# Performance work log

Measured on AMD Instinct MI355X. Metric: run time of the kernel, lower is better.

## Reference

```python
import jax, jax.numpy as jnp
import numpy as np
import math

D_MODEL = 1024
NUM_HEADS = 16
NUM_LAYERS = 4
D_FF = 4096
TEXT_DIM = 512
B, SV, ST = 4, 2048, 100
EPS = 1e-5


def positional_encoding(seq_len, d):
    pos = jnp.arange(seq_len, dtype=jnp.float32)[:, None]
    div = jnp.exp(jnp.arange(0, d, 2, dtype=jnp.float32) * (-math.log(10000.0) / d))
    pe = jnp.zeros((seq_len, d), dtype=jnp.float32)
    pe = pe.at[:, 0::2].set(jnp.sin(pos * div))
    pe = pe.at[:, 1::2].set(jnp.cos(pos * div))
    return pe  # [seq_len, d]


def layer_norm(x, g, b):
    mu = jnp.mean(x, axis=-1, keepdims=True)
    var = jnp.mean(jnp.square(x - mu), axis=-1, keepdims=True)
    return (x - mu) * jax.lax.rsqrt(var + EPS) * g + b


def setup_inputs() -> dict:
    key = jax.random.key(0)
    ks = jax.random.split(key, 24)
    s = 0.02
    inp = {
        "video": jax.random.normal(ks[0], (B, SV, D_MODEL), jnp.float32),
        "text": jax.random.normal(ks[1], (B, ST, TEXT_DIM), jnp.float32),
        "text_mask": jnp.ones((B, ST), jnp.int32),
        # stacked per-layer params, weights stored [in, out]
        "Wq_w": jax.random.normal(ks[2], (NUM_LAYERS, D_MODEL, D_MODEL)) * s,
        "Wq_b": jnp.zeros((NUM_LAYERS, D_MODEL)),
        "Wk_w": jax.random.normal(ks[3], (NUM_LAYERS, TEXT_DIM, D_MODEL)) * s,
        "Wk_b": jnp.zeros((NUM_LAYERS, D_MODEL)),
        "Wv_w": jax.random.normal(ks[4], (NUM_LAYERS, TEXT_DIM, D_MODEL)) * s,
        "Wv_b": jnp.zeros((NUM_LAYERS, D_MODEL)),
        "Wo_w": jax.random.normal(ks[5], (NUM_LAYERS, D_MODEL, D_MODEL)) * s,
        "Wo_b": jnp.zeros((NUM_LAYERS, D_MODEL)),
        "fc1_w": jax.random.normal(ks[6], (NUM_LAYERS, D_MODEL, D_FF)) * s,
        "fc1_b": jnp.zeros((NUM_LAYERS, D_FF)),
        "fc2_w": jax.random.normal(ks[7], (NUM_LAYERS, D_FF, D_MODEL)) * s,
        "fc2_b": jnp.zeros((NUM_LAYERS, D_MODEL)),
        "n2_g": jnp.ones((NUM_LAYERS, D_MODEL)),
        "n2_b": jnp.zeros((NUM_LAYERS, D_MODEL)),
        "n3_g": jnp.ones((NUM_LAYERS, D_MODEL)),
        "n3_b": jnp.zeros((NUM_LAYERS, D_MODEL)),
    }
    return inp


def cross_attn_layer(video, text, mask, wq, bq, wk, bk, wv, bv, wo, bo):
    Bv, Sq, D = video.shape
    H, dk = NUM_HEADS, D_MODEL // NUM_HEADS
    q = (video @ wq + bq).reshape(Bv, Sq, H, dk).transpose(0, 2, 1, 3)  # bhqd
    k = (text @ wk + bk).reshape(Bv, -1, H, dk).transpose(0, 2, 1, 3)   # bhkd
    v = (text @ wv + bv).reshape(Bv, -1, H, dk).transpose(0, 2, 1, 3)
    scores = jnp.einsum("bhqd,bhkd->bhqk", q, k) / math.sqrt(dk)
    scores = jnp.where(mask, scores, jnp.float32(-1e9))
    probs = jax.nn.softmax(scores, axis=-1)
    out = jnp.einsum("bhqk,bhkd->bhqd", probs, v)
    out = out.transpose(0, 2, 1, 3).reshape(Bv, Sq, D)
    return out @ wo + bo


def reference(video, text, text_mask, Wq_w, Wq_b, Wk_w, Wk_b, Wv_w, Wv_b,
              Wo_w, Wo_b, fc1_w, fc1_b, fc2_w, fc2_b, n2_g, n2_b, n3_g, n3_b):
    video = video + positional_encoding(SV, D_MODEL)[None, :video.shape[1]]
    text = text + positional_encoding(ST, TEXT_DIM)[None, :text.shape[1]]
    mask = (text_mask != 0)[:, None, None, :]  # [B,1,1,St]
    for l in range(NUM_LAYERS):
        attn = cross_attn_layer(video, text, mask,
                                Wq_w[l], Wq_b[l], Wk_w[l], Wk_b[l],
                                Wv_w[l], Wv_b[l], Wo_w[l], Wo_b[l])
        video = layer_norm(video + attn, n2_g[l], n2_b[l])
        ff = jax.nn.relu(video @ fc1_w[l] + fc1_b[l]) @ fc2_w[l] + fc2_b[l]
        video = layer_norm(video + ff, n3_g[l], n3_b[l])
    return video
```

## Files before the change

### kernel.cpp

```cpp
#include <hip/hip_runtime.h>
#include <cstdint>
#include <cstddef>

typedef unsigned short u16;
typedef __attribute__((ext_vector_type(8))) __bf16 bf16x8;
typedef __attribute__((ext_vector_type(4))) float f32x4;

__device__ __forceinline__ f32x4 mfma_16x16x32(bf16x8 a, bf16x8 b, f32x4 c) {
  return __builtin_amdgcn_mfma_f32_16x16x32_bf16(a, b, c, 0, 0, 0);
}

__device__ __forceinline__ u16 f2bf(float f) {
  union { float f; uint32_t u; } c; c.f = f;
  uint32_t u = c.u + 0x7FFFu + ((c.u >> 16) & 1u);
  return (u16)(u >> 16);
}

__device__ __forceinline__ float bf2f(u16 x) {
  union { uint32_t u; float f; } c; c.u = ((uint32_t)x) << 16;
  return c.f;
}

__device__ __forceinline__ void gload_lds16(const void* g, void* l) {
  __builtin_amdgcn_global_load_lds(
      (__attribute__((address_space(1))) void*)(uintptr_t)g,
      (__attribute__((address_space(3))) void*)l, 16, 0, 0);
}

template<bool OUT_BF16, bool RELU, bool ACC>
__global__ __launch_bounds__(256, 2) void gemm_ring4(
    const u16* __restrict__ A, int lda, const u16* __restrict__ Bt, int ldb,
    const float* __restrict__ bias, void* Cout, int ldc,
    int M, int N, int K)
{
  constexpr int BM = 128, BN = 128;
  constexpr int SLOT = (BM + BN) * 32;
  __shared__ u16 ring[3 * SLOT];

  const int tid = threadIdx.x;
  const int lane = tid & 63, wave = tid >> 6;
  const int wm = wave >> 1, wn = wave & 1;
  const int m0 = blockIdx.x * BM, n0 = blockIdx.y * BN;

  const u16* gA[2];
  const u16* gB[2];
  #pragma unroll
  for (int i = 0; i < 2; i++) {
    int c = tid + i * 256, r = c >> 2;
    gA[i] = A + (size_t)(m0 + r) * lda + (((c & 3) ^ ((r >> 1) & 3)) * 8);
    gB[i] = Bt + (size_t)(n0 + r) * ldb + (((c & 3) ^ ((r >> 1) & 3)) * 8);
  }

  const int NK = K >> 5;

  auto STAGE = [&](int s, int ph) {
    u16* Sb = &ring[ph * SLOT];
    const int ko = s * 32;
    #pragma unroll
    for (int i = 0; i < 2; i++)
      gload_lds16(gA[i] + ko, Sb + (tid + i * 256) * 8);
    #pragma unroll
    for (int i = 0; i < 2; i++)
      gload_lds16(gB[i] + ko, Sb + BM * 32 + (tid + i * 256) * 8);
  };

  const int fr = lane & 15, g = lane >> 4;
  const int foff = fr * 32 + ((g ^ ((fr >> 1) & 3)) * 8);

  f32x4 acc[4][4];
  #pragma unroll
  for (int m = 0; m < 4; m++)
    #pragma unroll
    for (int n = 0; n < 4; n++) acc[m][n] = f32x4{0.f, 0.f, 0.f, 0.f};

  STAGE(0, 0);
  if (NK > 1) {
    STAGE(1, 1);
    asm volatile("s_waitcnt vmcnt(4)" ::: "memory");
  } else {
    asm volatile("s_waitcnt vmcnt(0)" ::: "memory");
  }
  __builtin_amdgcn_s_barrier();
  __builtin_amdgcn_sched_barrier(0);

  int phys = 0;
  for (int s = 0; s < NK; ++s) {
    const u16* As = &ring[phys * SLOT];
    const u16* Bs = As + BM * 32;

    bf16x8 bf[4];
    #pragma unroll
    for (int n = 0; n < 4; n++)
      bf[n] = *(const bf16x8*)(Bs + (wn * 64 + n * 16) * 32 + foff);
    bf16x8 af[4];
    #pragma unroll
    for (int m = 0; m < 4; m++)
      af[m] = *(const bf16x8*)(As + (wm * 64 + m * 16) * 32 + foff);

    if (s + 2 < NK) {
      int ph2 = phys + 2; if (ph2 >= 3) ph2 -= 3;
      STAGE(s + 2, ph2);
    }

    __builtin_amdgcn_s_setprio(1);
    #pragma unroll
    for (int m = 0; m < 4; m++)
      #pragma unroll
      for (int n = 0; n < 4; n++)
        acc[m][n] = mfma_16x16x32(af[m], bf[n], acc[m][n]);
    __builtin_amdgcn_s_setprio(0);

    if (s + 2 < NK) asm volatile("s_waitcnt vmcnt(4)" ::: "memory");
    else            asm volatile("s_waitcnt vmcnt(0)" ::: "memory");
    asm volatile("s_waitcnt lgkmcnt(0)" ::: "memory");
    __builtin_amdgcn_sched_barrier(0);
    __builtin_amdgcn_s_barrier();
    __builtin_amdgcn_sched_barrier(0);

    phys = phys + 1 == 3 ? 0 : phys + 1;
  }

  #pragma unroll
  for (int n = 0; n < 4; n++) {
    const int gcol = n0 + wn * 64 + n * 16 + fr;
    const float bv = bias ? bias[gcol] : 0.f;
    #pragma unroll
    for (int m = 0; m < 4; m++) {
      #pragma unroll
      for (int r = 0; r < 4; r++) {
        const int grow = m0 + wm * 64 + m * 16 + g * 4 + r;
        float v = acc[m][n][r] + bv;
        if (ACC) v += bf2f(((const u16*)Cout)[(size_t)grow * ldc + gcol]);
        if (RELU) v = fmaxf(v, 0.f);
        if (OUT_BF16) ((u16*)Cout)[(size_t)grow * ldc + gcol] = f2bf(v);
        else         ((float*)Cout)[(size_t)grow * ldc + gcol] = v;
      }
    }
  }
}

template<bool TRANS>
__global__ __launch_bounds__(256, 2) void gemm_bt(
    const u16* __restrict__ A, int lda, const u16* __restrict__ Bt, int ldb,
    const float* __restrict__ bias, u16* Cout, int ldc,
    int M, int N, int K)
{
  __shared__ u16 ldsA[128 * 32];
  __shared__ u16 ldsB[128 * 32];

  const int tid = threadIdx.x;
  const int lane = tid & 63, wave = tid >> 6;
  const int wr = wave >> 1, wc = wave & 1;
  const int m0 = blockIdx.x * 128, n0 = blockIdx.y * 128;

  const int c0 = tid, c1 = tid + 256;
  const int ar0 = c0 >> 2, ak0 = (c0 & 3) * 8;
  const int ar1 = c1 >> 2, ak1 = (c1 & 3) * 8;

  const bool av0 = (m0 + ar0) < M;
  const bool av1 = (m0 + ar1) < M;
  const u16* Ag0 = A + (size_t)(m0 + ar0) * lda + ak0;
  const u16* Ag1 = A + (size_t)(m0 + ar1) * lda + ak1;
  const u16* Bg0 = Bt + (size_t)(n0 + ar0) * ldb + ak0;
  const u16* Bg1 = Bt + (size_t)(n0 + ar1) * ldb + ak1;

  f32x4 acc[4][4] = {};
  const int fr = lane & 15, fo = (lane >> 4) * 8;

  for (int k0 = 0; k0 < K; k0 += 32) {
    if (av0) gload_lds16(Ag0 + k0, &ldsA[c0 * 8]);
    if (av1) gload_lds16(Ag1 + k0, &ldsA[c1 * 8]);
    gload_lds16(Bg0 + k0, &ldsB[c0 * 8]);
    gload_lds16(Bg1 + k0, &ldsB[c1 * 8]);
    asm volatile("s_waitcnt vmcnt(0)" ::: "memory");
    __syncthreads();

    bf16x8 af[4], bfr[4];
    #pragma unroll
    for (int m = 0; m < 4; m++)
      af[m] = *(const bf16x8*)&ldsA[(wr * 64 + m * 16 + fr) * 32 + fo];
    #pragma unroll
    for (int n = 0; n < 4; n++)
      bfr[n] = *(const bf16x8*)&ldsB[(wc * 64 + n * 16 + fr) * 32 + fo];
    #pragma unroll
    for (int m = 0; m < 4; m++)
      #pragma unroll
      for (int n = 0; n < 4; n++)
        acc[m][n] = mfma_16x16x32(af[m], bfr[n], acc[m][n]);
    __syncthreads();
  }

  const int g = lane >> 4;
  #pragma unroll
  for (int m = 0; m < 4; m++) {
    #pragma unroll
    for (int n = 0; n < 4; n++) {
      const int gcol = n0 + wc * 64 + n * 16 + fr;
      const float bv = bias[gcol];
      #pragma unroll
      for (int r = 0; r < 4; r++) {
        const int grow = m0 + wr * 64 + m * 16 + g * 4 + r;
        if (grow < M) {
          float v = acc[m][n][r] + bv;
          if (TRANS) {
            int bb = grow / 100, jj = grow - bb * 100;
            int h = gcol >> 6, d = gcol & 63;
            Cout[(size_t)(((bb * 16 + h) * 64 + d)) * 128 + jj] = f2bf(v);
          } else {
            Cout[(size_t)grow * ldc + gcol] = f2bf(v);
          }
        }
      }
    }
  }
}

__global__ void wconv_t(const float* __restrict__ src, u16* __restrict__ dst,
                        int K, int N)
{
  __shared__ float tile[32][33];
  const int n0 = blockIdx.x * 32, k0 = blockIdx.y * 32;
  const int tx = threadIdx.x, ty = threadIdx.y;
  #pragma unroll
  for (int i = 0; i < 4; i++)
    tile[ty + i * 8][tx] = src[(size_t)(k0 + ty + i * 8) * N + n0 + tx];
  __syncthreads();
  #pragma unroll
  for (int i = 0; i < 4; i++)
    dst[(size_t)(n0 + ty + i * 8) * K + k0 + tx] = f2bf(tile[tx][ty + i * 8]);
}

__global__ __launch_bounds__(256) void pe_video_k(const float* __restrict__ video,
                                                  u16* __restrict__ vbf)
{
  const int r = blockIdx.x;
  const int s = r & 2047;
  const int d0 = threadIdx.x * 4;
  const size_t base = (size_t)r * 1024 + d0;
  float4 v = *(const float4*)&video[base];
  const float coef = -9.210340371976184f / 1024.f;
  float o[4];
  float in[4] = {v.x, v.y, v.z, v.w};
  #pragma unroll
  for (int i = 0; i < 4; i++) {
    int d = d0 + i;
    int j = d >> 1;
    float dv = expf((float)(2 * j) * coef);
    float arg = (float)s * dv;
    float pe = (d & 1) ? cosf(arg) : sinf(arg);
    o[i] = in[i] + pe;
  }
  uint2 pk;
  pk.x = (uint32_t)f2bf(o[0]) | ((uint32_t)f2bf(o[1]) << 16);
  pk.y = (uint32_t)f2bf(o[2]) | ((uint32_t)f2bf(o[3]) << 16);
  *(uint2*)&vbf[base] = pk;
}

__global__ __launch_bounds__(128) void pe_text_k(const float* __restrict__ text,
                                                 u16* __restrict__ tbf)
{
  const int r = blockIdx.x;
  const int s = r % 100;
  const int d0 = threadIdx.x * 4;
  const size_t base = (size_t)r * 512 + d0;
  float4 v = *(const float4*)&text[base];
  const float coef = -9.210340371976184f / 512.f;
  float o[4];
  float in[4] = {v.x, v.y, v.z, v.w};
  #pragma unroll
  for (int i = 0; i < 4; i++) {
    int d = d0 + i;
    int j = d >> 1;
    float dv = expf((float)(2 * j) * coef);
    float arg = (float)s * dv;
    float pe = (d & 1) ? cosf(arg) : sinf(arg);
    o[i] = in[i] + pe;
  }
  uint2 pk;
  pk.x = (uint32_t)f2bf(o[0]) | ((uint32_t)f2bf(o[1]) << 16);
  pk.y = (uint32_t)f2bf(o[2]) | ((uint32_t)f2bf(o[3]) << 16);
  *(uint2*)&tbf[base] = pk;
}

template<bool LAST>
__global__ __launch_bounds__(256) void ln2(const u16* __restrict__ xin,
                                           const u16* __restrict__ delta,
                                           const float* __restrict__ gamma,
                                           const float* __restrict__ beta,
                                           u16* __restrict__ xbf,
                                           float* __restrict__ fout)
{
  const int row = blockIdx.x;
  const size_t base = (size_t)row * 1024;
  const int t = threadIdx.x;
  const int d0 = t * 4;
  uint2 xv = *(const uint2*)&xin[base + d0];
  uint2 dv = *(const uint2*)&delta[base + d0];
  float v0 = bf2f((u16)(xv.x & 0xFFFF)) + bf2f((u16)(dv.x & 0xFFFF));
  float v1 = bf2f((u16)(xv.x >> 16))    + bf2f((u16)(dv.x >> 16));
  float v2 = bf2f((u16)(xv.y & 0xFFFF)) + bf2f((u16)(dv.y & 0xFFFF));
  float v3 = bf2f((u16)(xv.y >> 16))    + bf2f((u16)(dv.y >> 16));
  float s = v0 + v1 + v2 + v3;
  float q = v0 * v0 + v1 * v1 + v2 * v2 + v3 * v3;
  #pragma unroll
  for (int d = 32; d >= 1; d >>= 1) { s += __shfl_xor(s, d); q += __shfl_xor(q, d); }
  __shared__ float red[8];
  const int lane = t & 63, w = t >> 6;
  if (lane == 0) { red[w] = s; red[4 + w] = q; }
  __syncthreads();
  float S = red[0] + red[1] + red[2] + red[3];
  float Qs = red[4] + red[5] + red[6] + red[7];
  const float mu = S * (1.f / 1024.f);
  const float var = Qs * (1.f / 1024.f) - mu * mu;
  const float rs = rsqrtf(var + 1e-5f);
  float4 gv = *(const float4*)&gamma[d0];
  float4 bv = *(const float4*)&beta[d0];
  float o0 = (v0 - mu) * rs * gv.x + bv.x;
  float o1 = (v1 - mu) * rs * gv.y + bv.y;
  float o2 = (v2 - mu) * rs * gv.z + bv.z;
  float o3 = (v3 - mu) * rs * gv.w + bv.w;
  if (LAST) {
    *(float4*)&fout[base + d0] = make_float4(o0, o1, o2, o3);
  } else {
    uint2 pk;
    pk.x = (uint32_t)f2bf(o0) | ((uint32_t)f2bf(o1) << 16);
    pk.y = (uint32_t)f2bf(o2) | ((uint32_t)f2bf(o3) << 16);
    *(uint2*)&xbf[base + d0] = pk;
  }
}

__global__ __launch_bounds__(256) void attn_v2(
    const u16* __restrict__ Q, const u16* __restrict__ Kb,
    const u16* __restrict__ Vtb, const int* __restrict__ mask,
    u16* __restrict__ Out)
{
  __shared__ u16 ldsP[64 * 136];

  const int tid = threadIdx.x, lane = tid & 63, w = tid >> 6;
  const int qb = blockIdx.x, bh = blockIdx.y;
  const int b = bh >> 4, h = bh & 15;
  const int fr = lane & 15, g = lane >> 4, fo = g * 8;

  const size_t qrow = (size_t)(b * 2048 + qb * 64 + w * 16 + fr) * 1024 + h * 64;
  bf16x8 qf0 = *(const bf16x8*)&Q[qrow + fo];
  bf16x8 qf1 = *(const bf16x8*)&Q[qrow + 32 + fo];

  float madd[7];
  #pragma unroll
  for (int t = 0; t < 7; t++) {
    int col = t * 16 + fr;
    int mv = (col < 100) ? mask[b * 100 + col] : 0;
    madd[t] = mv ? 0.f : -1e30f;
  }

  float sc[7][4];
  #pragma unroll
  for (int t = 0; t < 7; t++) {
    int col = t * 16 + fr;
    int jr = (col < 100) ? col : 99;
    const u16* kp = Kb + (size_t)(b * 100 + jr) * 1024 + h * 64;
    bf16x8 kf0 = *(const bf16x8*)&kp[fo];
    bf16x8 kf1 = *(const bf16x8*)&kp[32 + fo];
    f32x4 a = {};
    a = mfma_16x16x32(qf0, kf0, a);
    a = mfma_16x16x32(qf1, kf1, a);
    #pragma unroll
    for (int r = 0; r < 4; r++)
      sc[t][r] = a[r] * 0.125f + madd[t];
  }

  #pragma unroll
  for (int r = 0; r < 4; r++) {
    float m = sc[0][r];
    #pragma unroll
    for (int t = 1; t < 7; t++) m = fmaxf(m, sc[t][r]);
    #pragma unroll
    for (int d = 8; d >= 1; d >>= 1) m = fmaxf(m, __shfl_xor(m, d));
    float ssum = 0.f;
    #pragma unroll
    for (int t = 0; t < 7; t++) { float p = __expf(sc[t][r] - m); sc[t][r] = p; ssum += p; }
    #pragma unroll
    for (int d = 8; d >= 1; d >>= 1) ssum += __shfl_xor(ssum, d);
    float is = 1.f / ssum;
    #pragma unroll
    for (int t = 0; t < 7; t++)
      ldsP[(w * 16 + g * 4 + r) * 136 + t * 16 + fr] = f2bf(sc[t][r] * is);
  }
  {
    u16* zp = &ldsP[(w * 16 + fr) * 136 + 112 + g * 6];
    #pragma unroll
    for (int i = 0; i < 6; i++) zp[i] = 0;
  }

  bf16x8 pa[4];
  #pragma unroll
  for (int kk = 0; kk < 4; kk++)
    pa[kk] = *(const bf16x8*)&ldsP[(w * 16 + fr) * 136 + kk * 32 + fo];
  const u16* vtbase = Vtb + (size_t)bh * 64 * 128;
  #pragma unroll
  for (int nt = 0; nt < 4; nt++) {
    f32x4 a = {};
    #pragma unroll
    for (int kk = 0; kk < 4; kk++) {
      bf16x8 vf = *(const bf16x8*)&vtbase[(size_t)(nt * 16 + fr) * 128 + kk * 32 + fo];
      a = mfma_16x16x32(pa[kk], vf, a);
    }
    #pragma unroll
    for (int r = 0; r < 4; r++) {
      size_t orow = (size_t)(b * 2048 + qb * 64 + w * 16 + g * 4 + r) * 1024 + h * 64 + nt * 16 + fr;
      Out[orow] = f2bf(a[r]);
    }
  }
}

extern "C" void kernel_launch(void* const* d_in, const int* in_sizes, int n_in,
                              void* d_out, int out_size, void* d_ws, size_t ws_size,
                              hipStream_t stream) {
  const float* video = (const float*)d_in[0];
  const float* text  = (const float*)d_in[1];
  const int*   text_mask = (const int*)d_in[2];
  const float* Wq_w = (const float*)d_in[3];
  const float* Wq_b = (const float*)d_in[4];
  const float* Wk_w = (const float*)d_in[5];
  const float* Wk_b = (const float*)d_in[6];
  const float* Wv_w = (const float*)d_in[7];
  const float* Wv_b = (const float*)d_in[8];
  const float* Wo_w = (const float*)d_in[9];
  const float* Wo_b = (const float*)d_in[10];
  const float* fc1_w = (const float*)d_in[11];
  const float* fc1_b = (const float*)d_in[12];
  const float* fc2_w = (const float*)d_in[13];
  const float* fc2_b = (const float*)d_in[14];
  const float* n2_g = (const float*)d_in[15];
  const float* n2_b = (const float*)d_in[16];
  const float* n3_g = (const float*)d_in[17];
  const float* n3_b = (const float*)d_in[18];

  char* ws = (char*)d_ws;
  size_t off = 0;
  auto alloc = [&](size_t bytes) {
    char* p = ws + off;
    off += (bytes + 255) & ~(size_t)255;
    return p;
  };
  u16* vbf = (u16*)alloc((size_t)8192 * 1024 * 2);
  u16* tbf = (u16*)alloc((size_t)400 * 512 * 2);
  u16* wqT = (u16*)alloc((size_t)1024 * 1024 * 2);
  u16* wkT = (u16*)alloc((size_t)1024 * 512 * 2);
  u16* wvT = (u16*)alloc((size_t)1024 * 512 * 2);
  u16* woT = (u16*)alloc((size_t)1024 * 1024 * 2);
  u16* f1T = (u16*)alloc((size_t)4096 * 1024 * 2);
  u16* f2T = (u16*)alloc((size_t)1024 * 4096 * 2);
  char* S = alloc((size_t)35192832);
  u16* qbf  = (u16*)S;
  u16* kbf  = (u16*)(S + 16777216);
  u16* abf  = (u16*)(S + 16777216 + 1638400);
  u16* h1c  = (u16*)S;
  u16* vtb  = (u16*)alloc((size_t)64 * 64 * 128 * 2);
  u16* dbf  = (u16*)alloc((size_t)8192 * 1024 * 2);
  float* fout = (float*)d_out;

  hipMemsetAsync(vtb, 0, (size_t)64 * 64 * 128 * 2, stream);

  pe_video_k<<<8192, 256, 0, stream>>>(video, vbf);
  pe_text_k<<<400, 128, 0, stream>>>(text, tbf);

  dim3 tb(32, 8, 1);
  for (int l = 0; l < 4; ++l) {
    wconv_t<<<dim3(32, 32), tb, 0, stream>>>(Wq_w + (size_t)l * 1024 * 1024, wqT, 1024, 1024);
    wconv_t<<<dim3(32, 16), tb, 0, stream>>>(Wk_w + (size_t)l * 512 * 1024, wkT, 512, 1024);
    wconv_t<<<dim3(32, 16), tb, 0, stream>>>(Wv_w + (size_t)l * 512 * 1024, wvT, 512, 1024);
    wconv_t<<<dim3(32, 32), tb, 0, stream>>>(Wo_w + (size_t)l * 1024 * 1024, woT, 1024, 1024);
    wconv_t<<<dim3(128, 32), tb, 0, stream>>>(fc1_w + (size_t)l * 1024 * 4096, f1T, 1024, 4096);
    wconv_t<<<dim3(32, 128), tb, 0, stream>>>(fc2_w + (size_t)l * 4096 * 1024, f2T, 4096, 1024);

    gemm_ring4<true, false, false><<<dim3(64, 8), 256, 0, stream>>>(
        vbf, 1024, wqT, 1024, Wq_b + l * 1024, qbf, 1024, 8192, 1024, 1024);
    gemm_bt<false><<<dim3(4, 8), 256, 0, stream>>>(
        tbf, 512, wkT, 512, Wk_b + l * 1024, kbf, 1024, 400, 1024, 512);
    gemm_bt<true><<<dim3(4, 8), 256, 0, stream>>>(
        tbf, 512, wvT, 512, Wv_b + l * 1024, vtb, 1024, 400, 1024, 512);
    attn_v2<<<dim3(32, 64), 256, 0, stream>>>(qbf, kbf, vtb, text_mask, abf);
    gemm_ring4<true, false, false><<<dim3(64, 8), 256, 0, stream>>>(
        abf, 1024, woT, 1024, Wo_b + l * 1024, dbf, 1024, 8192, 1024, 1024);
    ln2<false><<<8192, 256, 0, stream>>>(vbf, dbf, n2_g + l * 1024, n2_b + l * 1024, vbf, nullptr);

    for (int c = 0; c < 2; ++c) {
      gemm_ring4<true, true, false><<<dim3(64, 16), 256, 0, stream>>>(
          vbf, 1024, f1T + (size_t)c * 2048 * 1024, 1024,
          fc1_b + l * 4096 + c * 2048, h1c, 2048, 8192, 2048, 1024);
      if (c == 0)
        gemm_ring4<true, false, false><<<dim3(64, 8), 256, 0, stream>>>(
            h1c, 2048, f2T + (size_t)c * 2048, 4096,
            fc2_b + l * 1024, dbf, 1024, 8192, 1024, 2048);
      else
        gemm_ring4<true, false, true><<<dim3(64, 8), 256, 0, stream>>>(
            h1c, 2048, f2T + (size_t)c * 2048, 4096,
            nullptr, dbf, 1024, 8192, 1024, 2048);
    }
    if (l == 3)
      ln2<true><<<8192, 256, 0, stream>>>(vbf, dbf, n3_g + l * 1024, n3_b + l * 1024, nullptr, fout);
    else
      ln2<false><<<8192, 256, 0, stream>>>(vbf, dbf, n3_g + l * 1024, n3_b + l * 1024, vbf, nullptr);
  }
}
```

Baseline: 1.358 ms.

## Replace GEMM with 256x128x64 eight-wave kernel using split-phase staged loads

The GEMM kernel grows from 128x128 tiles with 4 waves and BK=32 to 256x128 tiles with 8 waves and BK=64, in a three-buffer LDS ring with 8-way XOR swizzling. Each K-tile is split into four MFMA phases, and the global-to-LDS loads for tile t+2 are interleaved across those phases with barriers between them. The aim is more data reuse per loaded byte and finer overlap of loads with MFMA work. In exchange, LDS use grows to about 144KB per block and there are many more barriers per iteration, which may cut occupancy and add sync stalls.

New measurement: 1.336 ms. About the same (-1.6%).

```diff
diff --git a/kernel.cpp b/kernel.cpp
--- a/kernel.cpp
+++ b/kernel.cpp
@@ -28,44 +28,52 @@
 }
 
 template<bool OUT_BF16, bool RELU, bool ACC>
-__global__ __launch_bounds__(256, 2) void gemm_ring4(
+__global__ __launch_bounds__(512, 2) void gemm8p(
     const u16* __restrict__ A, int lda, const u16* __restrict__ Bt, int ldb,
     const float* __restrict__ bias, void* Cout, int ldc,
     int M, int N, int K)
 {
-  constexpr int BM = 128, BN = 128;
-  constexpr int SLOT = (BM + BN) * 32;
-  __shared__ u16 ring[3 * SLOT];
+  constexpr int BM = 256, BN = 128, BK = 64;
+  constexpr int TILE = (BM + BN) * BK;
+  __shared__ u16 lds[3 * TILE];
 
   const int tid = threadIdx.x;
   const int lane = tid & 63, wave = tid >> 6;
   const int wm = wave >> 1, wn = wave & 1;
   const int m0 = blockIdx.x * BM, n0 = blockIdx.y * BN;
 
-  const u16* gA[2];
+  const u16* gA[4];
   const u16* gB[2];
   #pragma unroll
+  for (int i = 0; i < 4; i++) {
+    int c = tid + i * 512, r = c >> 3, q = c & 7;
+    gA[i] = A + (size_t)(m0 + r) * lda + ((q ^ (r & 7)) * 8);
+  }
+  #pragma unroll
   for (int i = 0; i < 2; i++) {
-    int c = tid + i * 256, r = c >> 2;
-    gA[i] = A + (size_t)(m0 + r) * lda + (((c & 3) ^ ((r >> 1) & 3)) * 8);
-    gB[i] = Bt + (size_t)(n0 + r) * ldb + (((c & 3) ^ ((r >> 1) & 3)) * 8);
-  }
-
-  const int NK = K >> 5;
-
-  auto STAGE = [&](int s, int ph) {
-    u16* Sb = &ring[ph * SLOT];
-    const int ko = s * 32;
-    #pragma unroll
-    for (int i = 0; i < 2; i++)
-      gload_lds16(gA[i] + ko, Sb + (tid + i * 256) * 8);
-    #pragma unroll
-    for (int i = 0; i < 2; i++)
-      gload_lds16(gB[i] + ko, Sb + BM * 32 + (tid + i * 256) * 8);
+    int c = tid + i * 512, r = c >> 3, q = c & 7;
+    gB[i] = Bt + (size_t)(n0 + r) * ldb + ((q ^ (r & 7)) * 8);
+  }
+
+  const int NT = K >> 6;
+
+  auto STAGE = [&](int t, int buf, int piece) {
+    u16* Sb = &lds[buf * TILE];
+    const int ko = t * 64;
+    if (piece == 0) {
+      gload_lds16(gA[0] + ko, Sb + tid * 8);
+      gload_lds16(gA[1] + ko, Sb + (tid + 512) * 8);
+    } else if (piece == 1) {
+      gload_lds16(gA[2] + ko, Sb + (tid + 1024) * 8);
+      gload_lds16(gA[3] + ko, Sb + (tid + 1536) * 8);
+    } else {
+      gload_lds16(gB[0] + ko, Sb + BM * 64 + tid * 8);
+      gload_lds16(gB[1] + ko, Sb + BM * 64 + (tid + 512) * 8);
+    }
   };
 
   const int fr = lane & 15, g = lane >> 4;
-  const int foff = fr * 32 + ((g ^ ((fr >> 1) & 3)) * 8);
+  const int sx = fr & 7;
 
   f32x4 acc[4][4];
   #pragma unroll
@@ -73,63 +81,109 @@
     #pragma unroll
     for (int n = 0; n < 4; n++) acc[m][n] = f32x4{0.f, 0.f, 0.f, 0.f};
 
-  STAGE(0, 0);
-  if (NK > 1) {
-    STAGE(1, 1);
-    asm volatile("s_waitcnt vmcnt(4)" ::: "memory");
-  } else {
-    asm volatile("s_waitcnt vmcnt(0)" ::: "memory");
-  }
+  STAGE(0, 0, 0); STAGE(0, 0, 1); STAGE(0, 0, 2);
+  STAGE(1, 1, 0); STAGE(1, 1, 1); STAGE(1, 1, 2);
+  asm volatile("s_waitcnt vmcnt(6)" ::: "memory");
   __builtin_amdgcn_s_barrier();
   __builtin_amdgcn_sched_barrier(0);
 
-  int phys = 0;
-  for (int s = 0; s < NK; ++s) {
-    const u16* As = &ring[phys * SLOT];
-    const u16* Bs = As + BM * 32;
-
-    bf16x8 bf[4];
-    #pragma unroll
-    for (int n = 0; n < 4; n++)
-      bf[n] = *(const bf16x8*)(Bs + (wn * 64 + n * 16) * 32 + foff);
-    bf16x8 af[4];
-    #pragma unroll
-    for (int m = 0; m < 4; m++)
-      af[m] = *(const bf16x8*)(As + (wm * 64 + m * 16) * 32 + foff);
-
-    if (s + 2 < NK) {
-      int ph2 = phys + 2; if (ph2 >= 3) ph2 -= 3;
-      STAGE(s + 2, ph2);
-    }
-
-    __builtin_amdgcn_s_setprio(1);
-    #pragma unroll
-    for (int m = 0; m < 4; m++)
-      #pragma unroll
-      for (int n = 0; n < 4; n++)
-        acc[m][n] = mfma_16x16x32(af[m], bf[n], acc[m][n]);
-    __builtin_amdgcn_s_setprio(0);
-
-    if (s + 2 < NK) asm volatile("s_waitcnt vmcnt(4)" ::: "memory");
-    else            asm volatile("s_waitcnt vmcnt(0)" ::: "memory");
+  int cur = 0;
+  for (int t = 0; t < NT; ++t) {
+    const u16* As = &lds[cur * TILE];
+    const u16* Bs = As + BM * 64;
+    const bool st = (t + 2 < NT);
+    int sbuf = cur + 2; if (sbuf >= 3) sbuf -= 3;
+
+    bf16x8 bf[4], afA[2], afB[2];
+    const int arow0 = wm * 64 + fr;
+    const int brow0 = wn * 64 + fr;
+
+    #pragma unroll
+    for (int nf = 0; nf < 4; nf++)
+      bf[nf] = *(const bf16x8*)(Bs + (brow0 + nf * 16) * 64 + ((g ^ sx) * 8));
+    #pragma unroll
+    for (int mf = 0; mf < 2; mf++)
+      afA[mf] = *(const bf16x8*)(As + (arow0 + mf * 16) * 64 + ((g ^ sx) * 8));
+    if (st) STAGE(t + 2, sbuf, 0);
+    __builtin_amdgcn_s_barrier();
     asm volatile("s_waitcnt lgkmcnt(0)" ::: "memory");
     __builtin_amdgcn_sched_barrier(0);
-    __builtin_amdgcn_s_barrier();
+    __builtin_amdgcn_s_setprio(1);
+    #pragma unroll
+    for (int mf = 0; mf < 2; mf++)
+      #pragma unroll
+      for (int nf = 0; nf < 4; nf++)
+        acc[mf][nf] = mfma_16x16x32(afA[mf], bf[nf], acc[mf][nf]);
+    __builtin_amdgcn_s_setprio(0);
+    __builtin_amdgcn_s_barrier();
+
+    #pragma unroll
+    for (int mf = 0; mf < 2; mf++)
+      afB[mf] = *(const bf16x8*)(As + (arow0 + (mf + 2) * 16) * 64 + ((g ^ sx) * 8));
+    if (st) STAGE(t + 2, sbuf, 1);
+    __builtin_amdgcn_s_barrier();
+    asm volatile("s_waitcnt lgkmcnt(0)" ::: "memory");
     __builtin_amdgcn_sched_barrier(0);
-
-    phys = phys + 1 == 3 ? 0 : phys + 1;
-  }
-
-  #pragma unroll
-  for (int n = 0; n < 4; n++) {
-    const int gcol = n0 + wn * 64 + n * 16 + fr;
+    __builtin_amdgcn_s_setprio(1);
+    #pragma unroll
+    for (int mf = 0; mf < 2; mf++)
+      #pragma unroll
+      for (int nf = 0; nf < 4; nf++)
+        acc[mf + 2][nf] = mfma_16x16x32(afB[mf], bf[nf], acc[mf + 2][nf]);
+    __builtin_amdgcn_s_setprio(0);
+    __builtin_amdgcn_s_barrier();
+
+    #pragma unroll
+    for (int nf = 0; nf < 4; nf++)
+      bf[nf] = *(const bf16x8*)(Bs + (brow0 + nf * 16) * 64 + (((4 + g) ^ sx) * 8));
+    #pragma unroll
+    for (int mf = 0; mf < 2; mf++)
+      afA[mf] = *(const bf16x8*)(As + (arow0 + mf * 16) * 64 + (((4 + g) ^ sx) * 8));
+    if (st) STAGE(t + 2, sbuf, 2);
+    __builtin_amdgcn_s_barrier();
+    asm volatile("s_waitcnt lgkmcnt(0)" ::: "memory");
+    __builtin_amdgcn_sched_barrier(0);
+    __builtin_amdgcn_s_setprio(1);
+    #pragma unroll
+    for (int mf = 0; mf < 2; mf++)
+      #pragma unroll
+      for (int nf = 0; nf < 4; nf++)
+        acc[mf][nf] = mfma_16x16x32(afA[mf], bf[nf], acc[mf][nf]);
+    __builtin_amdgcn_s_setprio(0);
+    __builtin_amdgcn_s_barrier();
+
+    #pragma unroll
+    for (int mf = 0; mf < 2; mf++)
+      afB[mf] = *(const bf16x8*)(As + (arow0 + (mf + 2) * 16) * 64 + (((4 + g) ^ sx) * 8));
+    __builtin_amdgcn_s_barrier();
+    asm volatile("s_waitcnt lgkmcnt(0)" ::: "memory");
+    __builtin_amdgcn_sched_barrier(0);
+    __builtin_amdgcn_s_setprio(1);
+    #pragma unroll
+    for (int mf = 0; mf < 2; mf++)
+      #pragma unroll
+      for (int nf = 0; nf < 4; nf++)
+        acc[mf + 2][nf] = mfma_16x16x32(afB[mf], bf[nf], acc[mf + 2][nf]);
+    __builtin_amdgcn_s_setprio(0);
+    if (st) asm volatile("s_waitcnt vmcnt(6)" ::: "memory");
+    else    asm volatile("s_waitcnt vmcnt(0)" ::: "memory");
+    __builtin_amdgcn_sched_barrier(0);
+    __builtin_amdgcn_s_barrier();
+    __builtin_amdgcn_sched_barrier(0);
+
+    cur = cur + 1 == 3 ? 0 : cur + 1;
+  }
+
+  #pragma unroll
+  for (int nf = 0; nf < 4; nf++) {
+    const int gcol = n0 + wn * 64 + nf * 16 + fr;
     const float bv = bias ? bias[gcol] : 0.f;
     #pragma unroll
-    for (int m = 0; m < 4; m++) {
+    for (int mf = 0; mf < 4; mf++) {
       #pragma unroll
       for (int r = 0; r < 4; r++) {
-        const int grow = m0 + wm * 64 + m * 16 + g * 4 + r;
-        float v = acc[m][n][r] + bv;
+        const int grow = m0 + wm * 64 + mf * 16 + g * 4 + r;
+        float v = acc[mf][nf][r] + bv;
         if (ACC) v += bf2f(((const u16*)Cout)[(size_t)grow * ldc + gcol]);
         if (RELU) v = fmaxf(v, 0.f);
         if (OUT_BF16) ((u16*)Cout)[(size_t)grow * ldc + gcol] = f2bf(v);
@@ -474,27 +528,27 @@
     wconv_t<<<dim3(128, 32), tb, 0, stream>>>(fc1_w + (size_t)l * 1024 * 4096, f1T, 1024, 4096);
     wconv_t<<<dim3(32, 128), tb, 0, stream>>>(fc2_w + (size_t)l * 4096 * 1024, f2T, 4096, 1024);
 
-    gemm_ring4<true, false, false><<<dim3(64, 8), 256, 0, stream>>>(
+    gemm8p<true, false, false><<<dim3(32, 8), 512, 0, stream>>>(
         vbf, 1024, wqT, 1024, Wq_b + l * 1024, qbf, 1024, 8192, 1024, 1024);
     gemm_bt<false><<<dim3(4, 8), 256, 0, stream>>>(
         tbf, 512, wkT, 512, Wk_b + l * 1024, kbf, 1024, 400, 1024, 512);
     gemm_bt<true><<<dim3(4, 8), 256, 0, stream>>>(
         tbf, 512, wvT, 512, Wv_b + l * 1024, vtb, 1024, 400, 1024, 512);
     attn_v2<<<dim3(32, 64), 256, 0, stream>>>(qbf, kbf, vtb, text_mask, abf);
-    gemm_ring4<true, false, false><<<dim3(64, 8), 256, 0, stream>>>(
+    gemm8p<true, false, false><<<dim3(32, 8), 512, 0, stream>>>(
         abf, 1024, woT, 1024, Wo_b + l * 1024, dbf, 1024, 8192, 1024, 1024);
     ln2<false><<<8192, 256, 0, stream>>>(vbf, dbf, n2_g + l * 1024, n2_b + l * 1024, vbf, nullptr);
 
     for (int c = 0; c < 2; ++c) {
-      gemm_ring4<true, true, false><<<dim3(64, 16), 256, 0, stream>>>(
+      gemm8p<true, true, false><<<dim3(32, 16), 512, 0, stream>>>(
           vbf, 1024, f1T + (size_t)c * 2048 * 1024, 1024,
           fc1_b + l * 4096 + c * 2048, h1c, 2048, 8192, 2048, 1024);
       if (c == 0)
-        gemm_ring4<true, false, false><<<dim3(64, 8), 256, 0, stream>>>(
+        gemm8p<true, false, false><<<dim3(32, 8), 512, 0, stream>>>(
             h1c, 2048, f2T + (size_t)c * 2048, 4096,
             fc2_b + l * 1024, dbf, 1024, 8192, 1024, 2048);
       else
-        gemm_ring4<true, false, true><<<dim3(64, 8), 256, 0, stream>>>(
+        gemm8p<true, false, true><<<dim3(32, 8), 512, 0, stream>>>(
             h1c, 2048, f2T + (size_t)c * 2048, 4096,
             nullptr, dbf, 1024, 8192, 1024, 2048);
     }
```
